# Kernel optimization log

Measured on AMD Instinct MI355X. Metric: run time of the kernel, lower is better.

## Reference

```python
import jax, jax.numpy as jnp
import numpy as np

B, T, N, H = 16, 49, 24, 256
S = 0.05  # init scale (keeps sigmoids/tanh out of saturation for numeric testing)


def setup_inputs() -> dict:
    key = jax.random.key(0)
    ks = jax.random.split(key, 16)
    rn = lambda k, shp: (jax.random.normal(k, shp, dtype=jnp.float32) * S)
    return dict(
        h=rn(ks[0], (B, T, N, H)),
        c_h=rn(ks[1], (B, T, N, H)),
        p=rn(ks[2], (B, T, N, H)),
        g_t=rn(ks[3], (B, T, N, H)),
        c_g_t=rn(ks[4], (B, T, N, H)),
        g_s=rn(ks[5], (B, T, N, H)),
        c_g_s=rn(ks[6], (B, T, N, H)),
        # 9 h-gates stacked in order: i, lt, ft, rt, s, gt, gs, o, c
        U=rn(ks[7], (9, N, H, H)),
        Wt=rn(ks[8], (9, N, 3 * H, H)),
        Ws=rn(ks[9], (9, N, H, H)),
        Zt=rn(ks[10], (9, N, H, H)),
        Zs=rn(ks[11], (9, N, H, H)),
        b=rn(ks[12], (9, N, 1, H)),
        # 6 global gates stacked in order: gtf, gtg, gto, gsf, gsg, gso
        Wg=rn(ks[13], (6, N, H, H)),
        Zg=rn(ks[14], (6, N, H, H)),
        bg=rn(ks[15], (6, N, 1, H)),
        train=1,
    )


def _cell(h, c_h, p, g_t, c_g_t, g_s, c_g_s, U, Wt, Ws, Zt, Zs, b, Wg, Zg, bg):
    pad_t = jnp.zeros_like(h[:, :, :1, :])
    pad_s = jnp.zeros_like(h[:, :1, :, :])
    # spatial (bone) neighbours along axis 2
    h_t_before = jnp.concatenate([pad_t, h[:, :, :-1, :]], axis=2)
    h_t_after = jnp.concatenate([h[:, :, 1:, :], pad_t], axis=2)
    h_tba = jnp.concatenate([h_t_before, h, h_t_after], axis=3)  # [B,T,N,3H]
    c_t_before = jnp.concatenate([pad_t, c_h[:, :, :-1, :]], axis=2)
    c_t_after = jnp.concatenate([c_h[:, :, 1:, :], pad_t], axis=2)
    # temporal predecessor along axis 1
    h_s_before = jnp.concatenate([pad_s, h[:, :-1, :, :]], axis=1)
    c_s_before = jnp.concatenate([pad_s, c_h[:, :-1, :, :]], axis=1)

    # Faithful quirk of the source: f_ft gate uses Zslt (the lt gate's Zs) for its g_s term.
    Zs_eff = Zs.at[2].set(Zs[1])

    # All 9 gate preactivations in one fused batched-GEMM pass: [9,B,T,N,H]
    pre = (jnp.einsum('btnh,gnhk->gbtnk', p, U)
           + jnp.einsum('btnm,gnmk->gbtnk', h_tba, Wt)
           + jnp.einsum('btnh,gnhk->gbtnk', h_s_before, Ws)
           + jnp.einsum('btnh,gnhk->gbtnk', g_t, Zt)
           + jnp.einsum('btnh,gnhk->gbtnk', g_s, Zs_eff)
           + b[:, None, None, :, 0, :])
    i_n, f_lt, f_ft, f_rt, f_s, f_gt, f_gs, o_n = jax.nn.sigmoid(pre[:8])
    c_n = jnp.tanh(pre[8])

    c_h_new = (f_lt * c_t_before + f_ft * c_h + f_rt * c_t_after
               + f_s * c_s_before + f_gt * c_g_t + f_gs * c_g_s + i_n * c_n)
    h_new = o_n * jnp.tanh(c_h_new)

    def _global(x_g, c_g, Wg3, Zg3, bg3):
        pre_g = (jnp.einsum('btnh,gnhk->gbtnk', h_new, Wg3)
                 + jnp.einsum('btnh,gnhk->gbtnk', x_g, Zg3)
                 + bg3[:, None, None, :, 0, :])
        f_g = jax.nn.sigmoid(pre_g[0])
        cand = jnp.tanh(pre_g[1])
        o_g = jax.nn.sigmoid(pre_g[2])
        c_g_new = f_g * c_g + (1.0 - f_g) * cand
        return o_g * jnp.tanh(c_g_new), c_g_new

    g_t_new, c_g_t_new = _global(g_t, c_g_t, Wg[:3], Zg[:3], bg[:3])
    g_s_new, c_g_s_new = _global(g_s, c_g_s, Wg[3:], Zg[3:], bg[3:])
    return h_new, c_h_new, g_t_new, c_g_t_new, g_s_new, c_g_s_new


def reference(h, c_h, p, g_t, c_g_t, g_s, c_g_s, U, Wt, Ws, Zt, Zs, b, Wg, Zg, bg, train):
    # `train` is a flag unused by the cell's math (kept for signature fidelity)
    return _cell(h, c_h, p, g_t, c_g_t, g_s, c_g_s, U, Wt, Ws, Zt, Zs, b, Wg, Zg, bg)
```

## Files before the change

kernel.cpp:

```cpp
#include <hip/hip_runtime.h>
#include <hip/hip_bf16.h>

typedef unsigned short u16;
typedef u16 u16x8 __attribute__((ext_vector_type(8)));
typedef short s16x8 __attribute__((ext_vector_type(8)));
typedef float f32x4 __attribute__((ext_vector_type(4)));
typedef unsigned int u32;

#define NN 24
#define TT 49
#define MR 784
#define SZT 4816896

__device__ inline u16 f2b(float f){
    __hip_bfloat16 b = __float2bfloat16(f); u16 r; __builtin_memcpy(&r, &b, 2); return r;
}
__device__ inline float sig_(float x){ return 1.f / (1.f + __expf(-x)); }
__device__ inline float tanh_(float x){ float e = __expf(2.f * x); return (e - 1.f) / (e + 1.f); }

#define WT0_ELEMS ((size_t)216 * 256 * 1792)
#define WT1_ELEMS ((size_t)144 * 256 * 512)
#define WS_NEED   ((WT0_ELEMS + WT1_ELEMS) * 2)

__global__ __launch_bounds__(256) void wprep0(
    const float* __restrict__ U,  const float* __restrict__ Wt,
    const float* __restrict__ Ws, const float* __restrict__ Zt,
    const float* __restrict__ Zs, u16* __restrict__ out)
{
    __shared__ u16 T[64][72];
    const int tid = threadIdx.x;
    const int kt = blockIdx.x, ct = blockIdx.y, z = blockIdx.z;
    const int n = z % NN, g = z / NN;
    const int k0 = kt * 64;

    const float* wbase;
    if (k0 < 256)       wbase = U  + (size_t)((g * NN + n) * 256 + k0)          * 256;
    else if (k0 < 1024) wbase = Wt + (size_t)((g * NN + n) * 768 + (k0 - 256))  * 256;
    else if (k0 < 1280) wbase = Ws + (size_t)((g * NN + n) * 256 + (k0 - 1024)) * 256;
    else if (k0 < 1536) wbase = Zt + (size_t)((g * NN + n) * 256 + (k0 - 1280)) * 256;
    else { const int g2 = (g == 2) ? 1 : g;
           wbase = Zs + (size_t)((g2 * NN + n) * 256 + (k0 - 1536)) * 256; }

    const int colg = ct * 64 + (tid & 15) * 4;
    #pragma unroll
    for (int it = 0; it < 4; ++it) {
        const int krl = (tid >> 4) + it * 16;
        const float4 v = *(const float4*)(wbase + (size_t)krl * 256 + colg);
        const int cl = (tid & 15) * 4;
        T[cl + 0][krl] = f2b(v.x); T[cl + 1][krl] = f2b(v.y);
        T[cl + 2][krl] = f2b(v.z); T[cl + 3][krl] = f2b(v.w);
    }
    __syncthreads();
    const int col_l = tid >> 2, ks = (tid & 3) * 16;
    const int ktile = 2 * kt + (ks >> 5);
    const int koff  = ks & 31;
    u16* dst = out + (size_t)z * 458752 + (size_t)ktile * 8192
                   + (size_t)(ct * 64 + col_l) * 32 + koff;
    u16x8 w0, w1;
    #pragma unroll
    for (int j = 0; j < 8; ++j) { w0[j] = T[col_l][ks + j]; w1[j] = T[col_l][ks + 8 + j]; }
    *(u16x8*)(dst) = w0; *(u16x8*)(dst + 8) = w1;
}

__global__ __launch_bounds__(256) void wprep1(
    const float* __restrict__ Wg, const float* __restrict__ Zg, u16* __restrict__ out)
{
    __shared__ u16 T[64][72];
    const int tid = threadIdx.x;
    const int kt = blockIdx.x, ct = blockIdx.y, z = blockIdx.z;
    const int k0 = kt * 64;
    const float* wbase = (k0 < 256)
        ? Wg + (size_t)(z * 256 + k0) * 256
        : Zg + (size_t)(z * 256 + (k0 - 256)) * 256;

    const int colg = ct * 64 + (tid & 15) * 4;
    #pragma unroll
    for (int it = 0; it < 4; ++it) {
        const int krl = (tid >> 4) + it * 16;
        const float4 v = *(const float4*)(wbase + (size_t)krl * 256 + colg);
        const int cl = (tid & 15) * 4;
        T[cl + 0][krl] = f2b(v.x); T[cl + 1][krl] = f2b(v.y);
        T[cl + 2][krl] = f2b(v.z); T[cl + 3][krl] = f2b(v.w);
    }
    __syncthreads();
    const int col_l = tid >> 2, ks = (tid & 3) * 16;
    const int ktile = 2 * kt + (ks >> 5);
    const int koff  = ks & 31;
    u16* dst = out + (size_t)z * 131072 + (size_t)ktile * 8192
                   + (size_t)(ct * 64 + col_l) * 32 + koff;
    u16x8 w0, w1;
    #pragma unroll
    for (int j = 0; j < 8; ++j) { w0[j] = T[col_l][ks + j]; w1[j] = T[col_l][ks + 8 + j]; }
    *(u16x8*)(dst) = w0; *(u16x8*)(dst + 8) = w1;
}

#define AB2 2048
#define BB2 18432

__global__ __launch_bounds__(256, 2) void fused_cell2(
    const float* __restrict__ p,   const float* __restrict__ h,
    const float* __restrict__ c_h, const float* __restrict__ g_t,
    const float* __restrict__ c_g_t, const float* __restrict__ g_s,
    const float* __restrict__ c_g_s,
    const u16* __restrict__ WT0, const float* __restrict__ Bias,
    float* __restrict__ h_new, float* __restrict__ c_h_new)
{
    extern __shared__ u16 smem[];

    const int tid = threadIdx.x;
    const int lin = blockIdx.x;
    const int xcd = lin & 7, j = lin >> 3;
    const int mtile = j % 13;
    const int slab  = (j / 13) * 8 + xcd;
    const int ntile = slab & 3, n = slab >> 2;

    const int s_r = tid >> 2, s_c = tid & 3;
    const int gr  = mtile * 64 + s_r;
    const bool mval = (gr < MR);
    const int ec = (gr * NN + n) * 256;
    const bool vnb = (n > 0), vna = (n < NN - 1), vtp = (gr % TT) != 0;

    const int wro = s_r * 32 + ((s_c ^ ((s_r >> 1) & 3)) << 3);
    const size_t bgo = (size_t)(ntile * 64 + s_r) * 32 + s_c * 8;

    const int wave = tid >> 6, lane = tid & 63;
    const int lrow = lane & 15, lci = lane >> 4;

    int aro[4];
    #pragma unroll
    for (int m = 0; m < 4; ++m) {
        const int row = m * 16 + lrow;
        aro[m] = row * 32 + ((lci ^ ((row >> 1) & 3)) << 3);
    }
    const int colr = wave * 16 + lrow;
    const int bro  = colr * 32 + ((lci ^ ((colr >> 1) & 3)) << 3);

    f32x4 acc[9][4];
    #pragma unroll
    for (int g = 0; g < 9; ++g)
        #pragma unroll
        for (int m = 0; m < 4; ++m) acc[g][m] = f32x4{0.f, 0.f, 0.f, 0.f};

    float4 alo, ahi; u16x8 brw[9];

    auto loadA = [&](int kt) {
        const int K0 = kt * 32, seg = K0 >> 8, koff = (K0 & 255) + s_c * 8;
        const float* src = nullptr; bool valid = mval;
        switch (seg) {
            case 0: src = p + ec + koff; break;
            case 1: valid &= vnb; src = h + ec - 256 + koff; break;
            case 2: src = h + ec + koff; break;
            case 3: valid &= vna; src = h + ec + 256 + koff; break;
            case 4: valid &= vtp; src = h + ec - NN * 256 + koff; break;
            case 5: src = g_t + ec + koff; break;
            default: src = g_s + ec + koff; break;
        }
        alo = make_float4(0.f, 0.f, 0.f, 0.f); ahi = alo;
        if (valid) { alo = *(const float4*)src; ahi = *(const float4*)(src + 4); }
    };
    auto loadB = [&](int kt) {
        const u16* wb = WT0 + (size_t)n * 458752 + (size_t)kt * 8192 + bgo;
        #pragma unroll
        for (int g = 0; g < 9; ++g)
            brw[g] = *(const u16x8*)(wb + (size_t)g * 11010048);
    };
    auto store = [&](int buf) {
        u16* Asb = smem + buf * AB2;
        u16* Bsb = smem + 2 * AB2 + buf * BB2;
        u16x8 aw;
        aw[0] = f2b(alo.x); aw[1] = f2b(alo.y); aw[2] = f2b(alo.z); aw[3] = f2b(alo.w);
        aw[4] = f2b(ahi.x); aw[5] = f2b(ahi.y); aw[6] = f2b(ahi.z); aw[7] = f2b(ahi.w);
        *(u16x8*)(&Asb[wro]) = aw;
        #pragma unroll
        for (int g = 0; g < 9; ++g)
            *(u16x8*)(&Bsb[g * 2048 + wro]) = brw[g];
    };
    auto domfma = [&](int buf) {
        const u16* Asb = smem + buf * AB2;
        const u16* Bsb = smem + 2 * AB2 + buf * BB2;
        s16x8 af[4];
        #pragma unroll
        for (int m = 0; m < 4; ++m) af[m] = *(const s16x8*)(&Asb[aro[m]]);
        #pragma unroll
        for (int g = 0; g < 9; ++g) {
            const s16x8 bf = *(const s16x8*)(&Bsb[g * 2048 + bro]);
            #pragma unroll
            for (int m = 0; m < 4; ++m)
                acc[g][m] = __builtin_amdgcn_mfma_f32_16x16x32_bf16(af[m], bf, acc[g][m], 0, 0, 0);
        }
    };

    loadA(0); loadB(0); store(0);
    for (int kt = 0; kt < 56; kt += 2) {
        __syncthreads();
        loadA(kt + 1); loadB(kt + 1);
        domfma(0);
        store(1);
        __syncthreads();
        if (kt + 2 < 56) { loadA(kt + 2); loadB(kt + 2); }
        domfma(1);
        if (kt + 2 < 56) store(0);
    }

    const int col = ntile * 64 + wave * 16 + lrow;
    float bv[9];
    #pragma unroll
    for (int g = 0; g < 9; ++g) bv[g] = Bias[(g * NN + n) * 256 + col];

    #pragma unroll
    for (int m = 0; m < 4; ++m) {
        #pragma unroll
        for (int i = 0; i < 4; ++i) {
            const int row = mtile * 64 + m * 16 + (lane >> 4) * 4 + i;
            if (row < MR) {
                const size_t e = ((size_t)(row * NN + n)) * 256 + col;
                const float i_n  = sig_(acc[0][m][i] + bv[0]);
                const float f_lt = sig_(acc[1][m][i] + bv[1]);
                const float f_ft = sig_(acc[2][m][i] + bv[2]);
                const float f_rt = sig_(acc[3][m][i] + bv[3]);
                const float f_s  = sig_(acc[4][m][i] + bv[4]);
                const float f_gt = sig_(acc[5][m][i] + bv[5]);
                const float f_gs = sig_(acc[6][m][i] + bv[6]);
                const float o_n  = sig_(acc[7][m][i] + bv[7]);
                const float c_n  = tanh_(acc[8][m][i] + bv[8]);
                const float cb = (n > 0)      ? c_h[e - 256] : 0.f;
                const float ca = (n < NN - 1) ? c_h[e + 256] : 0.f;
                const float cs = (row % TT)   ? c_h[e - NN * 256] : 0.f;
                const float cn = f_lt * cb + f_ft * c_h[e] + f_rt * ca
                               + f_s * cs + f_gt * c_g_t[e] + f_gs * c_g_s[e]
                               + i_n * c_n;
                c_h_new[e] = cn;
                h_new[e]   = o_n * tanh_(cn);
            }
        }
    }
}

__global__ __launch_bounds__(256, 3) void fused_global2(
    const float* __restrict__ hn,   const float* __restrict__ g_t,
    const float* __restrict__ g_s,  const float* __restrict__ c_g_t,
    const float* __restrict__ c_g_s,
    const u16* __restrict__ WT1, const float* __restrict__ Bg,
    float* __restrict__ out2, float* __restrict__ out3,
    float* __restrict__ out4, float* __restrict__ out5)
{
    __shared__ u16 smem[2 * 2048 + 2 * 6144];

    const int tid = threadIdx.x;
    const int lin = blockIdx.x;
    const int xcd = lin & 7, j = lin >> 3;
    const int mtile = j % 13;
    const int slab  = (j / 13) * 8 + xcd;
    const int ntile = slab & 3;
    const int zz    = slab >> 2;
    const int n = zz % NN, grp = zz / NN;

    const float* xg = grp ? g_s : g_t;
    const float* cg = grp ? c_g_s : c_g_t;
    float* og  = grp ? out4 : out2;
    float* ocg = grp ? out5 : out3;

    const int s_r = tid >> 2, s_c = tid & 3;
    const int gr  = mtile * 64 + s_r;
    const bool mval = (gr < MR);
    const int ec = (gr * NN + n) * 256;

    const int wro = s_r * 32 + ((s_c ^ ((s_r >> 1) & 3)) << 3);
    const size_t bgo = (size_t)(ntile * 64 + s_r) * 32 + s_c * 8;

    const int wave = tid >> 6, lane = tid & 63;
    const int lrow = lane & 15, lci = lane >> 4;

    int aro[4];
    #pragma unroll
    for (int m = 0; m < 4; ++m) {
        const int row = m * 16 + lrow;
        aro[m] = row * 32 + ((lci ^ ((row >> 1) & 3)) << 3);
    }
    const int colr = wave * 16 + lrow;
    const int bro  = colr * 32 + ((lci ^ ((colr >> 1) & 3)) << 3);

    f32x4 acc[3][4];
    #pragma unroll
    for (int g = 0; g < 3; ++g)
        #pragma unroll
        for (int m = 0; m < 4; ++m) acc[g][m] = f32x4{0.f, 0.f, 0.f, 0.f};

    float4 alo, ahi; u16x8 brw[3];

    auto loadA = [&](int kt) {
        const int K0 = kt * 32, koff = (K0 & 255) + s_c * 8;
        const float* src = ((K0 < 256) ? hn : xg) + ec + koff;
        alo = make_float4(0.f, 0.f, 0.f, 0.f); ahi = alo;
        if (mval) { alo = *(const float4*)src; ahi = *(const float4*)(src + 4); }
    };
    auto loadB = [&](int kt) {
        const u16* wb = WT1 + (size_t)(grp * 3 * NN + n) * 131072
                            + (size_t)kt * 8192 + bgo;
        #pragma unroll
        for (int g = 0; g < 3; ++g)
            brw[g] = *(const u16x8*)(wb + (size_t)g * 3145728);
    };
    auto store = [&](int buf) {
        u16* Asb = smem + buf * 2048;
        u16* Bsb = smem + 2 * 2048 + buf * 6144;
        u16x8 aw;
        aw[0] = f2b(alo.x); aw[1] = f2b(alo.y); aw[2] = f2b(alo.z); aw[3] = f2b(alo.w);
        aw[4] = f2b(ahi.x); aw[5] = f2b(ahi.y); aw[6] = f2b(ahi.z); aw[7] = f2b(ahi.w);
        *(u16x8*)(&Asb[wro]) = aw;
        #pragma unroll
        for (int g = 0; g < 3; ++g)
            *(u16x8*)(&Bsb[g * 2048 + wro]) = brw[g];
    };
    auto domfma = [&](int buf) {
        const u16* Asb = smem + buf * 2048;
        const u16* Bsb = smem + 2 * 2048 + buf * 6144;
        s16x8 af[4];
        #pragma unroll
        for (int m = 0; m < 4; ++m) af[m] = *(const s16x8*)(&Asb[aro[m]]);
        #pragma unroll
        for (int g = 0; g < 3; ++g) {
            const s16x8 bf = *(const s16x8*)(&Bsb[g * 2048 + bro]);
            #pragma unroll
            for (int m = 0; m < 4; ++m)
                acc[g][m] = __builtin_amdgcn_mfma_f32_16x16x32_bf16(af[m], bf, acc[g][m], 0, 0, 0);
        }
    };

    loadA(0); loadB(0); store(0);
    for (int kt = 0; kt < 16; kt += 2) {
        __syncthreads();
        loadA(kt + 1); loadB(kt + 1);
        domfma(0);
        store(1);
        __syncthreads();
        if (kt + 2 < 16) { loadA(kt + 2); loadB(kt + 2); }
        domfma(1);
        if (kt + 2 < 16) store(0);
    }

    const int col = ntile * 64 + wave * 16 + lrow;
    float bv[3];
    #pragma unroll
    for (int g = 0; g < 3; ++g) bv[g] = Bg[((grp * 3 + g) * NN + n) * 256 + col];

    #pragma unroll
    for (int m = 0; m < 4; ++m) {
        #pragma unroll
        for (int i = 0; i < 4; ++i) {
            const int row = mtile * 64 + m * 16 + (lane >> 4) * 4 + i;
            if (row < MR) {
                const size_t e = ((size_t)(row * NN + n)) * 256 + col;
                const float f    = sig_(acc[0][m][i] + bv[0]);
                const float cand = tanh_(acc[1][m][i] + bv[1]);
                const float o    = sig_(acc[2][m][i] + bv[2]);
                const float cn = f * cg[e] + (1.f - f) * cand;
                ocg[e] = cn;
                og[e]  = o * tanh_(cn);
            }
        }
    }
}

extern "C" void kernel_launch(void* const* d_in, const int* in_sizes, int n_in,
                              void* d_out, int out_size, void* d_ws, size_t ws_size,
                              hipStream_t stream)
{
    const float* h     = (const float*)d_in[0];
    const float* c_h   = (const float*)d_in[1];
    const float* p     = (const float*)d_in[2];
    const float* g_t   = (const float*)d_in[3];
    const float* c_g_t = (const float*)d_in[4];
    const float* g_s   = (const float*)d_in[5];
    const float* c_g_s = (const float*)d_in[6];
    const float* U     = (const float*)d_in[7];
    const float* Wt    = (const float*)d_in[8];
    const float* Ws    = (const float*)d_in[9];
    const float* Zt    = (const float*)d_in[10];
    const float* Zs    = (const float*)d_in[11];
    const float* bb    = (const float*)d_in[12];
    const float* Wg    = (const float*)d_in[13];
    const float* Zg    = (const float*)d_in[14];
    const float* bg    = (const float*)d_in[15];

    float* out0 = (float*)d_out;
    float* out1 = out0 + (size_t)SZT;
    float* out2 = out1 + (size_t)SZT;
    float* out3 = out2 + (size_t)SZT;
    float* out4 = out3 + (size_t)SZT;
    float* out5 = out4 + (size_t)SZT;

    u16* wt0 = (u16*)d_ws;
    u16* wt1 = wt0 + WT0_ELEMS;

    dim3 blk(256);
    wprep0<<<dim3(28, 4, 216), blk, 0, stream>>>(U, Wt, Ws, Zt, Zs, wt0);
    wprep1<<<dim3(8, 4, 144), blk, 0, stream>>>(Wg, Zg, wt1);

    hipFuncSetAttribute((const void*)fused_cell2,
                        hipFuncAttributeMaxDynamicSharedMemorySize, 81920);
    fused_cell2<<<dim3(1248), blk, 81920, stream>>>(
        p, h, c_h, g_t, c_g_t, g_s, c_g_s, wt0, bb, out0, out1);
    fused_global2<<<dim3(2496), blk, 0, stream>>>(
        out0, g_t, g_s, c_g_t, c_g_s, wt1, bg, out2, out3, out4, out5);
}
```

Before: 522.5 us.

## Load weight fragments straight from global into registers, skipping LDS staging

Result: slower. 541.3 us (+3.6%).

```diff
diff --git a/kernel.cpp b/kernel.cpp
--- a/kernel.cpp
+++ b/kernel.cpp
@@ -20,7 +20,6 @@
 
 #define WT0_ELEMS ((size_t)216 * 256 * 1792)
 #define WT1_ELEMS ((size_t)144 * 256 * 512)
-#define WS_NEED   ((WT0_ELEMS + WT1_ELEMS) * 2)
 
 __global__ __launch_bounds__(256) void wprep0(
     const float* __restrict__ U,  const float* __restrict__ Wt,
@@ -94,10 +93,7 @@
     *(u16x8*)(dst) = w0; *(u16x8*)(dst + 8) = w1;
 }
 
-#define AB2 2048
-#define BB2 18432
-
-__global__ __launch_bounds__(256, 2) void fused_cell2(
+__global__ __launch_bounds__(256, 2) void fused_cell3(
     const float* __restrict__ p,   const float* __restrict__ h,
     const float* __restrict__ c_h, const float* __restrict__ g_t,
     const float* __restrict__ c_g_t, const float* __restrict__ g_s,
@@ -105,7 +101,7 @@
     const u16* __restrict__ WT0, const float* __restrict__ Bias,
     float* __restrict__ h_new, float* __restrict__ c_h_new)
 {
-    extern __shared__ u16 smem[];
+    __shared__ u16 As[2][2048];
 
     const int tid = threadIdx.x;
     const int lin = blockIdx.x;
@@ -121,7 +117,6 @@
     const bool vnb = (n > 0), vna = (n < NN - 1), vtp = (gr % TT) != 0;
 
     const int wro = s_r * 32 + ((s_c ^ ((s_r >> 1) & 3)) << 3);
-    const size_t bgo = (size_t)(ntile * 64 + s_r) * 32 + s_c * 8;
 
     const int wave = tid >> 6, lane = tid & 63;
     const int lrow = lane & 15, lci = lane >> 4;
@@ -132,8 +127,8 @@
         const int row = m * 16 + lrow;
         aro[m] = row * 32 + ((lci ^ ((row >> 1) & 3)) << 3);
     }
-    const int colr = wave * 16 + lrow;
-    const int bro  = colr * 32 + ((lci ^ ((colr >> 1) & 3)) << 3);
+    const size_t bfo = (size_t)(ntile * 64 + wave * 16 + lrow) * 32 + lci * 8;
+    const u16* wbase = WT0 + (size_t)n * 458752 + bfo;
 
     f32x4 acc[9][4];
     #pragma unroll
@@ -141,7 +136,8 @@
         #pragma unroll
         for (int m = 0; m < 4; ++m) acc[g][m] = f32x4{0.f, 0.f, 0.f, 0.f};
 
-    float4 alo, ahi; u16x8 brw[9];
+    float4 alo, ahi;
+    s16x8 b0[9], b1[9];
 
     auto loadA = [&](int kt) {
         const int K0 = kt * 32, seg = K0 >> 8, koff = (K0 & 255) + s_c * 8;
@@ -158,48 +154,40 @@
         alo = make_float4(0.f, 0.f, 0.f, 0.f); ahi = alo;
         if (valid) { alo = *(const float4*)src; ahi = *(const float4*)(src + 4); }
     };
-    auto loadB = [&](int kt) {
-        const u16* wb = WT0 + (size_t)n * 458752 + (size_t)kt * 8192 + bgo;
-        #pragma unroll
-        for (int g = 0; g < 9; ++g)
-            brw[g] = *(const u16x8*)(wb + (size_t)g * 11010048);
-    };
-    auto store = [&](int buf) {
-        u16* Asb = smem + buf * AB2;
-        u16* Bsb = smem + 2 * AB2 + buf * BB2;
+    auto storeA = [&](int buf) {
         u16x8 aw;
         aw[0] = f2b(alo.x); aw[1] = f2b(alo.y); aw[2] = f2b(alo.z); aw[3] = f2b(alo.w);
         aw[4] = f2b(ahi.x); aw[5] = f2b(ahi.y); aw[6] = f2b(ahi.z); aw[7] = f2b(ahi.w);
-        *(u16x8*)(&Asb[wro]) = aw;
+        *(u16x8*)(&As[buf][wro]) = aw;
+    };
+    auto loadB = [&](int kt, s16x8 (&d)[9]) {
+        const u16* wb = wbase + (size_t)kt * 8192;
         #pragma unroll
         for (int g = 0; g < 9; ++g)
-            *(u16x8*)(&Bsb[g * 2048 + wro]) = brw[g];
-    };
-    auto domfma = [&](int buf) {
-        const u16* Asb = smem + buf * AB2;
-        const u16* Bsb = smem + 2 * AB2 + buf * BB2;
+            d[g] = *(const s16x8*)(wb + (size_t)g * 11010048);
+    };
+    auto domfma = [&](int buf, const s16x8 (&b)[9]) {
         s16x8 af[4];
         #pragma unroll
-        for (int m = 0; m < 4; ++m) af[m] = *(const s16x8*)(&Asb[aro[m]]);
-        #pragma unroll
-        for (int g = 0; g < 9; ++g) {
-            const s16x8 bf = *(const s16x8*)(&Bsb[g * 2048 + bro]);
+        for (int m = 0; m < 4; ++m) af[m] = *(const s16x8*)(&As[buf][aro[m]]);
+        #pragma unroll
+        for (int g = 0; g < 9; ++g)
             #pragma unroll
             for (int m = 0; m < 4; ++m)
-                acc[g][m] = __builtin_amdgcn_mfma_f32_16x16x32_bf16(af[m], bf, acc[g][m], 0, 0, 0);
-        }
-    };
-
-    loadA(0); loadB(0); store(0);
+                acc[g][m] = __builtin_amdgcn_mfma_f32_16x16x32_bf16(af[m], b[g], acc[g][m], 0, 0, 0);
+    };
+
+    loadA(0); storeA(0); loadB(0, b0);
+    __syncthreads();
     for (int kt = 0; kt < 56; kt += 2) {
+        loadA(kt + 1); loadB(kt + 1, b1);
+        domfma(0, b0);
+        storeA(1);
         __syncthreads();
-        loadA(kt + 1); loadB(kt + 1);
-        domfma(0);
-        store(1);
+        if (kt + 2 < 56) { loadA(kt + 2); loadB(kt + 2, b0); }
+        domfma(1, b1);
+        if (kt + 2 < 56) { storeA(0); }
         __syncthreads();
-        if (kt + 2 < 56) { loadA(kt + 2); loadB(kt + 2); }
-        domfma(1);
-        if (kt + 2 < 56) store(0);
     }
 
     const int col = ntile * 64 + wave * 16 + lrow;
@@ -236,7 +224,7 @@
     }
 }
 
-__global__ __launch_bounds__(256, 3) void fused_global2(
+__global__ __launch_bounds__(256, 4) void fused_global3(
     const float* __restrict__ hn,   const float* __restrict__ g_t,
     const float* __restrict__ g_s,  const float* __restrict__ c_g_t,
     const float* __restrict__ c_g_s,
@@ -244,7 +232,7 @@
     float* __restrict__ out2, float* __restrict__ out3,
     float* __restrict__ out4, float* __restrict__ out5)
 {
-    __shared__ u16 smem[2 * 2048 + 2 * 6144];
+    __shared__ u16 As[2][2048];
 
     const int tid = threadIdx.x;
     const int lin = blockIdx.x;
@@ -266,7 +254,6 @@
     const int ec = (gr * NN + n) * 256;
 
     const int wro = s_r * 32 + ((s_c ^ ((s_r >> 1) & 3)) << 3);
-    const size_t bgo = (size_t)(ntile * 64 + s_r) * 32 + s_c * 8;
 
     const int wave = tid >> 6, lane = tid & 63;
     const int lrow = lane & 15, lci = lane >> 4;
@@ -277,8 +264,8 @@
         const int row = m * 16 + lrow;
         aro[m] = row * 32 + ((lci ^ ((row >> 1) & 3)) << 3);
     }
-    const int colr = wave * 16 + lrow;
-    const int bro  = colr * 32 + ((lci ^ ((colr >> 1) & 3)) << 3);
+    const size_t bfo = (size_t)(ntile * 64 + wave * 16 + lrow) * 32 + lci * 8;
+    const u16* wbase = WT1 + (size_t)(grp * 3 * NN + n) * 131072 + bfo;
 
     f32x4 acc[3][4];
     #pragma unroll
@@ -286,7 +273,8 @@
         #pragma unroll
         for (int m = 0; m < 4; ++m) acc[g][m] = f32x4{0.f, 0.f, 0.f, 0.f};
 
-    float4 alo, ahi; u16x8 brw[3];
+    float4 alo, ahi;
+    s16x8 b0[3], b1[3];
 
     auto loadA = [&](int kt) {
         const int K0 = kt * 32, koff = (K0 & 255) + s_c * 8;
@@ -294,49 +282,40 @@
         alo = make_float4(0.f, 0.f, 0.f, 0.f); ahi = alo;
         if (mval) { alo = *(const float4*)src; ahi = *(const float4*)(src + 4); }
     };
-    auto loadB = [&](int kt) {
-        const u16* wb = WT1 + (size_t)(grp * 3 * NN + n) * 131072
-                            + (size_t)kt * 8192 + bgo;
-        #pragma unroll
-        for (int g = 0; g < 3; ++g)
-            brw[g] = *(const u16x8*)(wb + (size_t)g * 3145728);
-    };
-    auto store = [&](int buf) {
-        u16* Asb = smem + buf * 2048;
-        u16* Bsb = smem + 2 * 2048 + buf * 6144;
+    auto storeA = [&](int buf) {
         u16x8 aw;
         aw[0] = f2b(alo.x); aw[1] = f2b(alo.y); aw[2] = f2b(alo.z); aw[3] = f2b(alo.w);
         aw[4] = f2b(ahi.x); aw[5] = f2b(ahi.y); aw[6] = f2b(ahi.z); aw[7] = f2b(ahi.w);
-        *(u16x8*)(&Asb[wro]) = aw;
+        *(u16x8*)(&As[buf][wro]) = aw;
+    };
+    auto loadB = [&](int kt, s16x8 (&d)[3]) {
+        const u16* wb = wbase + (size_t)kt * 8192;
         #pragma unroll
         for (int g = 0; g < 3; ++g)
-            *(u16x8*)(&Bsb[g * 2048 + wro]) = brw[g];
-    };
-    auto domfma = [&](int buf) {
-        const u16* Asb = smem + buf * 2048;
-        const u16* Bsb = smem + 2 * 2048 + buf * 6144;
+            d[g] = *(const s16x8*)(wb + (size_t)g * 3145728);
+    };
+    auto domfma = [&](int buf, const s16x8 (&b)[3]) {
         s16x8 af[4];
         #pragma unroll
-        for (int m = 0; m < 4; ++m) af[m] = *(const s16x8*)(&Asb[aro[m]]);
-        #pragma unroll
-        for (int g = 0; g < 3; ++g) {
-            const s16x8 bf = *(const s16x8*)(&Bsb[g * 2048 + bro]);
+        for (int m = 0; m < 4; ++m) af[m] = *(const s16x8*)(&As[buf][aro[m]]);
+        #pragma unroll
+        for (int g = 0; g < 3; ++g)
             #pragma unroll
             for (int m = 0; m < 4; ++m)
-                acc[g][m] = __builtin_amdgcn_mfma_f32_16x16x32_bf16(af[m], bf, acc[g][m], 0, 0, 0);
-        }
-    };
-
-    loadA(0); loadB(0); store(0);
+                acc[g][m] = __builtin_amdgcn_mfma_f32_16x16x32_bf16(af[m], b[g], acc[g][m], 0, 0, 0);
+    };
+
+    loadA(0); storeA(0); loadB(0, b0);
+    __syncthreads();
     for (int kt = 0; kt < 16; kt += 2) {
+        loadA(kt + 1); loadB(kt + 1, b1);
+        domfma(0, b0);
+        storeA(1);
         __syncthreads();
-        loadA(kt + 1); loadB(kt + 1);
-        domfma(0);
-        store(1);
+        if (kt + 2 < 16) { loadA(kt + 2); loadB(kt + 2, b0); }
+        domfma(1, b1);
+        if (kt + 2 < 16) { storeA(0); }
         __syncthreads();
-        if (kt + 2 < 16) { loadA(kt + 2); loadB(kt + 2); }
-        domfma(1);
-        if (kt + 2 < 16) store(0);
     }
 
     const int col = ntile * 64 + wave * 16 + lrow;
@@ -397,10 +376,8 @@
     wprep0<<<dim3(28, 4, 216), blk, 0, stream>>>(U, Wt, Ws, Zt, Zs, wt0);
     wprep1<<<dim3(8, 4, 144), blk, 0, stream>>>(Wg, Zg, wt1);
 
-    hipFuncSetAttribute((const void*)fused_cell2,
-                        hipFuncAttributeMaxDynamicSharedMemorySize, 81920);
-    fused_cell2<<<dim3(1248), blk, 81920, stream>>>(
+    fused_cell3<<<dim3(1248), blk, 0, stream>>>(
         p, h, c_h, g_t, c_g_t, g_s, c_g_s, wt0, bb, out0, out1);
-    fused_global2<<<dim3(2496), blk, 0, stream>>>(
+    fused_global3<<<dim3(2496), blk, 0, stream>>>(
         out0, g_t, g_s, c_g_t, c_g_s, wt1, bg, out2, out3, out4, out5);
 }
```
